# Kernel optimization log

Measured on AMD Instinct MI355X. Metric: run time of the kernel, lower is better.

The kernel has to match this reference:

```python
import jax, jax.numpy as jnp
import numpy as np

N_NODES = 50000
N_EDGES = 800000
D_IN = 64
D_OUT = 64


def setup_inputs() -> dict:
    key = jax.random.key(0)
    k1, k2, k3, k4 = jax.random.split(key, 4)
    x = jax.random.normal(k1, (N_NODES, D_IN), dtype=jnp.float32)
    src = jax.random.randint(k2, (N_EDGES,), 0, N_NODES, dtype=jnp.int64)
    dst = jax.random.randint(k3, (N_EDGES,), 0, N_NODES, dtype=jnp.int64)
    W = jax.random.normal(k4, (D_IN, D_OUT), dtype=jnp.float32) / np.sqrt(D_IN)
    b = jnp.zeros((D_OUT,), dtype=jnp.float32)
    return {"x": x, "src": src, "dst": dst, "W": W, "b": b}


def reference(x, src, dst, W, b):
    # DGL GraphConv, norm='both': out = D_in^{-1/2} A D_out^{-1/2} x W + b
    n = x.shape[0]
    ones = jnp.ones(src.shape[0], dtype=x.dtype)
    out_deg = jax.ops.segment_sum(ones, src, num_segments=n)  # out-degree of each node
    in_deg = jax.ops.segment_sum(ones, dst, num_segments=n)   # in-degree of each node
    norm_src = jax.lax.rsqrt(jnp.clip(out_deg, 1.0))          # [N]
    norm_dst = jax.lax.rsqrt(jnp.clip(in_deg, 1.0))           # [N]
    h = x * norm_src[:, None]                                 # [N, D_in]
    msg = jnp.take(h, src, axis=0)                            # [E, D_in] gather
    agg = jax.ops.segment_sum(msg, dst, num_segments=n)       # [N, D_in] scatter-add
    agg = agg * norm_dst[:, None]
    return agg @ W + b                                        # [N, D_out]
```

## Files before the change

### kernel.cpp

```cpp
#include <hip/hip_runtime.h>
#include <hip/hip_fp16.h>

#define N_NODES 50000
#define N_EDGES 800000
#define D 64

#define SLICES 100
#define I4S    2000
#define NI4    200000
#define NWORDS 12512

typedef float vfloat2 __attribute__((ext_vector_type(2)));

#define CTR_OFF    0
#define META_OFF   256
#define SNORM_OFF  400384
#define SSRC_OFF   600576
#define OCC_OFF    3800576
#define PART_OFF   4600832
#define YA_OFF     14610432
#define YB_OFF     17810688

__global__ __launch_bounds__(256) void degree_occ_kernel(const int4* __restrict__ src4,
                                                         const int4* __restrict__ dst4,
                                                         unsigned int* __restrict__ partial,
                                                         uchar4* __restrict__ occ4,
                                                         int* __restrict__ ctr) {
    __shared__ unsigned int hist[NWORDS];
    int tid = threadIdx.x;
    if (blockIdx.x == 0 && tid == 0) *ctr = 0;
    uint4* h4 = (uint4*)hist;
    for (int i = tid; i < NWORDS / 4; i += 256) h4[i] = make_uint4(0, 0, 0, 0);
    __syncthreads();

    int role  = blockIdx.x & 1;
    int slice = blockIdx.x >> 1;
    int beg = slice * I4S, end = beg + I4S;
    if (role == 0) {
        for (int i = beg + tid; i < end; i += 256) {
            int4 v = src4[i];
            atomicAdd(&hist[v.x >> 2], 1u << ((v.x & 3) * 8));
            atomicAdd(&hist[v.y >> 2], 1u << ((v.y & 3) * 8));
            atomicAdd(&hist[v.z >> 2], 1u << ((v.z & 3) * 8));
            atomicAdd(&hist[v.w >> 2], 1u << ((v.w & 3) * 8));
        }
    } else {
        for (int i = beg + tid; i < end; i += 256) {
            int4 v = dst4[i];
            unsigned int o0 = (atomicAdd(&hist[v.x >> 2], 1u << ((v.x & 3) * 8)) >> ((v.x & 3) * 8)) & 0xFFu;
            unsigned int o1 = (atomicAdd(&hist[v.y >> 2], 1u << ((v.y & 3) * 8)) >> ((v.y & 3) * 8)) & 0xFFu;
            unsigned int o2 = (atomicAdd(&hist[v.z >> 2], 1u << ((v.z & 3) * 8)) >> ((v.z & 3) * 8)) & 0xFFu;
            unsigned int o3 = (atomicAdd(&hist[v.w >> 2], 1u << ((v.w & 3) * 8)) >> ((v.w & 3) * 8)) & 0xFFu;
            occ4[i] = make_uchar4((unsigned char)o0, (unsigned char)o1,
                                  (unsigned char)o2, (unsigned char)o3);
        }
    }
    __syncthreads();

    uint4* p4 = (uint4*)(partial + (size_t)blockIdx.x * NWORDS);
    for (int i = tid; i < NWORDS / 4; i += 256) p4[i] = h4[i];
}

__global__ __launch_bounds__(256) void merge_scan_kernel(unsigned int* __restrict__ partial,
                                                         int2* __restrict__ meta,
                                                         float* __restrict__ snorm,
                                                         int* __restrict__ ctr) {
    int w = blockIdx.x * blockDim.x + threadIdx.x;
    int lane = threadIdx.x & 63;
    unsigned int accin = 0, accout = 0;
    if (w < 12500) {
        unsigned int* po = partial + w;
        unsigned int* pd = partial + NWORDS + w;
#pragma unroll 4
        for (int s = 0; s < SLICES; s++) {
            size_t off = (size_t)(2 * s) * NWORDS;
            accout += po[off];
            unsigned int v = pd[off];
            pd[off] = accin;
            accin += v;
        }
    }
    int d0 = accin & 0xFF, d1 = (accin >> 8) & 0xFF,
        d2 = (accin >> 16) & 0xFF, d3 = (accin >> 24) & 0xFF;
    int tsum = d0 + d1 + d2 + d3;
    int run = tsum;
#pragma unroll
    for (int off = 1; off < 64; off <<= 1) {
        int v = __shfl_up(run, off);
        if (lane >= off) run += v;
    }
    int wtot = __shfl(run, 63);
    int wbase = 0;
    if (lane == 63) wbase = atomicAdd(ctr, wtot);
    wbase = __shfl(wbase, 63);
    if (w < 12500) {
        int b0 = wbase + run - tsum;
        int b1 = b0 + d0, b2 = b1 + d1, b3 = b2 + d2;
        ((int4*)meta)[2 * w]     = make_int4(b0, d0, b1, d1);
        ((int4*)meta)[2 * w + 1] = make_int4(b2, d2, b3, d3);
        int o0 = accout & 0xFF, o1 = (accout >> 8) & 0xFF,
            o2 = (accout >> 16) & 0xFF, o3 = (accout >> 24) & 0xFF;
        ((float4*)snorm)[w] = make_float4(rsqrtf(fmaxf((float)o0, 1.f)),
                                          rsqrtf(fmaxf((float)o1, 1.f)),
                                          rsqrtf(fmaxf((float)o2, 1.f)),
                                          rsqrtf(fmaxf((float)o3, 1.f)));
    }
}

#define FYBLK 1024
__global__ __launch_bounds__(256, 4) void filly_kernel(const int4* __restrict__ src4,
                                                       const int4* __restrict__ dst4,
                                                       const uchar4* __restrict__ occ4,
                                                       const unsigned int* __restrict__ partial,
                                                       const int2* __restrict__ meta,
                                                       int* __restrict__ ssrc,
                                                       const float* __restrict__ x,
                                                       const float* __restrict__ snorm,
                                                       const float* __restrict__ W,
                                                       __half* __restrict__ yA,
                                                       __half* __restrict__ yB) {
    int tid = blockIdx.x * blockDim.x + threadIdx.x;
    int lane = threadIdx.x & 63;

    if (tid < NI4) {
        int s = tid / I4S;
        const unsigned int* pref = partial + (size_t)(2 * s + 1) * NWORDS;
        int4 sv = src4[tid], tv = dst4[tid];
        uchar4 oc = occ4[tid];
#define FILL_ONE(T, S, O)                                                     \
        {                                                                     \
            int t = (T); int sh = (t & 3) * 8;                                \
            int p = meta[t].x + (int)((pref[t >> 2] >> sh) & 0xFFu) + (int)(O); \
            ssrc[p] = (S);                                                    \
        }
        FILL_ONE(tv.x, sv.x, oc.x)
        FILL_ONE(tv.y, sv.y, oc.y)
        FILL_ONE(tv.z, sv.z, oc.z)
        FILL_ONE(tv.w, sv.w, oc.w)
#undef FILL_ONE
    }

    float Wreg[D];
#pragma unroll
    for (int k = 0; k < D; k++) Wreg[k] = W[k * D + lane];
    __half* yh = (lane < 32) ? yA : yB;
    int jl = lane & 31;
    int wave = tid >> 6;
    const int nwaves = FYBLK * 4;
    for (int n = wave; n < N_NODES; n += nwaves) {
        float hv = x[(size_t)n * D + lane] * snorm[n];
        int hb = __float_as_int(hv);
        float p0 = 0.f, p1 = 0.f, p2 = 0.f, p3 = 0.f;
#pragma unroll
        for (int k = 0; k < D; k += 4) {
            p0 = fmaf(__int_as_float(__builtin_amdgcn_readlane(hb, k + 0)), Wreg[k + 0], p0);
            p1 = fmaf(__int_as_float(__builtin_amdgcn_readlane(hb, k + 1)), Wreg[k + 1], p1);
            p2 = fmaf(__int_as_float(__builtin_amdgcn_readlane(hb, k + 2)), Wreg[k + 2], p2);
            p3 = fmaf(__int_as_float(__builtin_amdgcn_readlane(hb, k + 3)), Wreg[k + 3], p3);
        }
        yh[(size_t)n * 32 + jl] = __float2half((p0 + p1) + (p2 + p3));
    }
}

#define GBLK 2048
__global__ __launch_bounds__(256, 8) void gather_kernel(const __half2* __restrict__ yA,
                                                        const __half2* __restrict__ yB,
                                                        const int* __restrict__ ssrc,
                                                        const int2* __restrict__ meta,
                                                        const float* __restrict__ bias,
                                                        float* __restrict__ out) {
    int lane = threadIdx.x & 63;
    int q = lane >> 4;
    int c = lane & 15;
    int pass = blockIdx.x & 1;
    int pblk = blockIdx.x >> 1;
    int wave = (pblk << 2) | (threadIdx.x >> 6);
    const int nwaves = (GBLK / 2) * 4;

    float2 b2 = ((const float2*)bias)[(pass << 4) + c];
    const __half2* ycol = (pass ? yB : yA) + c;

#define ACC(A, F) { (A).x += (F).x; (A).y += (F).y; }

    for (int n = wave; n < N_NODES; n += nwaves) {
        int2 m = meta[n];
        int beg = m.x, end = m.x + m.y;
        float dn = rsqrtf(fmaxf((float)m.y, 1.0f));
        float2 a0 = make_float2(0.f, 0.f), a1 = a0, a2 = a0, a3 = a0;
        float2 a4 = a0, a5 = a0, a6 = a0, a7 = a0;
        int i = beg;
        for (; i + 32 <= end; i += 32) {
            int s0 = ssrc[i + q],      s1 = ssrc[i + 4 + q];
            int s2 = ssrc[i + 8 + q],  s3 = ssrc[i + 12 + q];
            int s4 = ssrc[i + 16 + q], s5 = ssrc[i + 20 + q];
            int s6 = ssrc[i + 24 + q], s7 = ssrc[i + 28 + q];
            float2 f0 = __half22float2(ycol[(size_t)s0 * 16]);
            float2 f1 = __half22float2(ycol[(size_t)s1 * 16]);
            float2 f2 = __half22float2(ycol[(size_t)s2 * 16]);
            float2 f3 = __half22float2(ycol[(size_t)s3 * 16]);
            float2 f4 = __half22float2(ycol[(size_t)s4 * 16]);
            float2 f5 = __half22float2(ycol[(size_t)s5 * 16]);
            float2 f6 = __half22float2(ycol[(size_t)s6 * 16]);
            float2 f7 = __half22float2(ycol[(size_t)s7 * 16]);
            ACC(a0, f0) ACC(a1, f1) ACC(a2, f2) ACC(a3, f3)
            ACC(a4, f4) ACC(a5, f5) ACC(a6, f6) ACC(a7, f7)
        }
        for (; i + 16 <= end; i += 16) {
            int s0 = ssrc[i + q],      s1 = ssrc[i + 4 + q];
            int s2 = ssrc[i + 8 + q],  s3 = ssrc[i + 12 + q];
            float2 f0 = __half22float2(ycol[(size_t)s0 * 16]);
            float2 f1 = __half22float2(ycol[(size_t)s1 * 16]);
            float2 f2 = __half22float2(ycol[(size_t)s2 * 16]);
            float2 f3 = __half22float2(ycol[(size_t)s3 * 16]);
            ACC(a0, f0) ACC(a1, f1) ACC(a2, f2) ACC(a3, f3)
        }
        for (; i + 4 <= end; i += 4) {
            int s = ssrc[i + q];
            float2 f = __half22float2(ycol[(size_t)s * 16]);
            ACC(a0, f)
        }
        int rem = end - i;
        if (q < rem) {
            int s = ssrc[i + q];
            float2 f = __half22float2(ycol[(size_t)s * 16]);
            ACC(a1, f)
        }
        float2 t;
        t.x = ((a0.x + a1.x) + (a2.x + a3.x)) + ((a4.x + a5.x) + (a6.x + a7.x));
        t.y = ((a0.y + a1.y) + (a2.y + a3.y)) + ((a4.y + a5.y) + (a6.y + a7.y));
        t.x += __shfl(t.x, lane ^ 16); t.y += __shfl(t.y, lane ^ 16);
        t.x += __shfl(t.x, lane ^ 32); t.y += __shfl(t.y, lane ^ 32);
        if (q == 0) {
            vfloat2 o;
            o.x = fmaf(t.x, dn, b2.x);
            o.y = fmaf(t.y, dn, b2.y);
            __builtin_nontemporal_store(o, (vfloat2*)(out + (size_t)n * D + (pass << 5)) + c);
        }
    }
#undef ACC
}

extern "C" void kernel_launch(void* const* d_in, const int* in_sizes, int n_in,
                              void* d_out, int out_size, void* d_ws, size_t ws_size,
                              hipStream_t stream) {
    const float* x   = (const float*)d_in[0];
    const int*   src = (const int*)d_in[1];
    const int*   dst = (const int*)d_in[2];
    const float* W   = (const float*)d_in[3];
    const float* b   = (const float*)d_in[4];
    float* out = (float*)d_out;

    char* ws = (char*)d_ws;
    int*          ctr   = (int*)(ws + CTR_OFF);
    int2*         meta  = (int2*)(ws + META_OFF);
    float*        snorm = (float*)(ws + SNORM_OFF);
    int*          ssrc  = (int*)(ws + SSRC_OFF);
    uchar4*       occ4  = (uchar4*)(ws + OCC_OFF);
    unsigned int* part  = (unsigned int*)(ws + PART_OFF);
    __half*       yA    = (__half*)(ws + YA_OFF);
    __half*       yB    = (__half*)(ws + YB_OFF);

    const int4* src4 = (const int4*)src;
    const int4* dst4 = (const int4*)dst;

    degree_occ_kernel<<<2 * SLICES, 256, 0, stream>>>(src4, dst4, part, occ4, ctr);
    merge_scan_kernel<<<(12500 + 255) / 256, 256, 0, stream>>>(part, meta, snorm, ctr);
    filly_kernel<<<FYBLK, 256, 0, stream>>>(src4, dst4, occ4, part, meta, ssrc,
                                            x, snorm, W, yA, yB);
    gather_kernel<<<GBLK, 256, 0, stream>>>((const __half2*)yA, (const __half2*)yB,
                                            ssrc, meta, b, out);
}
```

Before: 151.6 us.

## Overlap x@W with degree histogram and move source norm into gather

The x@W projection no longer depends on the source degree norm. The per-source norm is now applied inside the gather as an FMA weight, which lets the projection run in extra blocks of the degree/histogram kernel at the same time as the histogramming. The merge-scan kernel now uses 4 threads per word, splitting the 100-slice prefix scan into halves across in and out, to get more parallelism. The cost is an extra snorm gather per edge in the gather kernel and a lone projection that competes for the same launch as the LDS-heavy histogram blocks.

```diff
diff --git a/kernel.cpp b/kernel.cpp
--- a/kernel.cpp
+++ b/kernel.cpp
@@ -9,6 +9,9 @@
 #define I4S    2000
 #define NI4    200000
 #define NWORDS 12512
+#define HBLK   200
+#define ZBLK   568
+#define DEGZ_BLOCKS (HBLK + ZBLK)
 
 typedef float vfloat2 __attribute__((ext_vector_type(2)));
 
@@ -18,16 +21,46 @@
 #define SSRC_OFF   600576
 #define OCC_OFF    3800576
 #define PART_OFF   4600832
-#define YA_OFF     14610432
-#define YB_OFF     17810688
-
-__global__ __launch_bounds__(256) void degree_occ_kernel(const int4* __restrict__ src4,
-                                                         const int4* __restrict__ dst4,
-                                                         unsigned int* __restrict__ partial,
-                                                         uchar4* __restrict__ occ4,
-                                                         int* __restrict__ ctr) {
+#define ZA_OFF     14610432
+#define ZB_OFF     17810688
+
+__global__ __launch_bounds__(256) void degz_kernel(const int4* __restrict__ src4,
+                                                   const int4* __restrict__ dst4,
+                                                   unsigned int* __restrict__ partial,
+                                                   uchar4* __restrict__ occ4,
+                                                   int* __restrict__ ctr,
+                                                   const float* __restrict__ x,
+                                                   const float* __restrict__ W,
+                                                   __half* __restrict__ zA,
+                                                   __half* __restrict__ zB) {
     __shared__ unsigned int hist[NWORDS];
     int tid = threadIdx.x;
+
+    if (blockIdx.x >= HBLK) {
+        int lane = tid & 63;
+        float Wreg[D];
+#pragma unroll
+        for (int k = 0; k < D; k++) Wreg[k] = W[k * D + lane];
+        __half* zh = (lane < 32) ? zA : zB;
+        int jl = lane & 31;
+        int wave = (blockIdx.x - HBLK) * 4 + (tid >> 6);
+        const int nwaves = ZBLK * 4;
+        for (int n = wave; n < N_NODES; n += nwaves) {
+            float hv = x[(size_t)n * D + lane];
+            int hb = __float_as_int(hv);
+            float p0 = 0.f, p1 = 0.f, p2 = 0.f, p3 = 0.f;
+#pragma unroll
+            for (int k = 0; k < D; k += 4) {
+                p0 = fmaf(__int_as_float(__builtin_amdgcn_readlane(hb, k + 0)), Wreg[k + 0], p0);
+                p1 = fmaf(__int_as_float(__builtin_amdgcn_readlane(hb, k + 1)), Wreg[k + 1], p1);
+                p2 = fmaf(__int_as_float(__builtin_amdgcn_readlane(hb, k + 2)), Wreg[k + 2], p2);
+                p3 = fmaf(__int_as_float(__builtin_amdgcn_readlane(hb, k + 3)), Wreg[k + 3], p3);
+            }
+            zh[(size_t)n * 32 + jl] = __float2half((p0 + p1) + (p2 + p3));
+        }
+        return;
+    }
+
     if (blockIdx.x == 0 && tid == 0) *ctr = 0;
     uint4* h4 = (uint4*)hist;
     for (int i = tid; i < NWORDS / 4; i += 256) h4[i] = make_uint4(0, 0, 0, 0);
@@ -61,29 +94,55 @@
     for (int i = tid; i < NWORDS / 4; i += 256) p4[i] = h4[i];
 }
 
+#define MSBLK 196
 __global__ __launch_bounds__(256) void merge_scan_kernel(unsigned int* __restrict__ partial,
                                                          int2* __restrict__ meta,
                                                          float* __restrict__ snorm,
                                                          int* __restrict__ ctr) {
-    int w = blockIdx.x * blockDim.x + threadIdx.x;
     int lane = threadIdx.x & 63;
-    unsigned int accin = 0, accout = 0;
-    if (w < 12500) {
-        unsigned int* po = partial + w;
-        unsigned int* pd = partial + NWORDS + w;
-#pragma unroll 4
-        for (int s = 0; s < SLICES; s++) {
-            size_t off = (size_t)(2 * s) * NWORDS;
-            accout += po[off];
-            unsigned int v = pd[off];
-            pd[off] = accin;
-            accin += v;
-        }
-    }
+    int r = threadIdx.x & 3;
+    int w = (blockIdx.x * blockDim.x + threadIdx.x) >> 2;
+    bool act = (w < 12500);
+
+    unsigned int buf[50];
+    unsigned int acc = 0;
+    if (act) {
+        int isdst = (r >= 2);
+        int sbase = (r & 1) ? 50 : 0;
+        unsigned int* p = partial + (size_t)isdst * NWORDS
+                        + (size_t)(2 * sbase) * NWORDS + w;
+#pragma unroll
+        for (int s = 0; s < 50; s++) {
+            unsigned int v = p[(size_t)(2 * s) * NWORDS];
+            buf[s] = v;
+            if (r == 2) p[(size_t)(2 * s) * NWORDS] = acc;
+            acc += v;
+        }
+    }
+    unsigned int mysum = acc;
+
+    int wl = lane & ~3;
+    unsigned int s0v = __shfl(mysum, wl);
+    unsigned int s1v = __shfl(mysum, wl | 1);
+    unsigned int s2v = __shfl(mysum, wl | 2);
+    unsigned int s3v = __shfl(mysum, wl | 3);
+
+    if (act && r == 3) {
+        unsigned int* p = partial + NWORDS + (size_t)(2 * 50) * NWORDS + w;
+        unsigned int a2 = s2v;
+#pragma unroll
+        for (int s = 0; s < 50; s++) {
+            p[(size_t)(2 * s) * NWORDS] = a2;
+            a2 += buf[s];
+        }
+    }
+
+    unsigned int accin  = s2v + s3v;
+    unsigned int accout = s0v + s1v;
     int d0 = accin & 0xFF, d1 = (accin >> 8) & 0xFF,
         d2 = (accin >> 16) & 0xFF, d3 = (accin >> 24) & 0xFF;
     int tsum = d0 + d1 + d2 + d3;
-    int run = tsum;
+    int run = (act && r == 3) ? tsum : 0;
 #pragma unroll
     for (int off = 1; off < 64; off <<= 1) {
         int v = __shfl_up(run, off);
@@ -93,7 +152,8 @@
     int wbase = 0;
     if (lane == 63) wbase = atomicAdd(ctr, wtot);
     wbase = __shfl(wbase, 63);
-    if (w < 12500) {
+
+    if (act && r == 3) {
         int b0 = wbase + run - tsum;
         int b1 = b0 + d0, b2 = b1 + d1, b3 = b2 + d2;
         ((int4*)meta)[2 * w]     = make_int4(b0, d0, b1, d1);
@@ -107,66 +167,37 @@
     }
 }
 
-#define FYBLK 1024
-__global__ __launch_bounds__(256, 4) void filly_kernel(const int4* __restrict__ src4,
-                                                       const int4* __restrict__ dst4,
-                                                       const uchar4* __restrict__ occ4,
-                                                       const unsigned int* __restrict__ partial,
-                                                       const int2* __restrict__ meta,
-                                                       int* __restrict__ ssrc,
-                                                       const float* __restrict__ x,
-                                                       const float* __restrict__ snorm,
-                                                       const float* __restrict__ W,
-                                                       __half* __restrict__ yA,
-                                                       __half* __restrict__ yB) {
+__global__ __launch_bounds__(256) void fill_kernel(const int4* __restrict__ src4,
+                                                   const int4* __restrict__ dst4,
+                                                   const uchar4* __restrict__ occ4,
+                                                   const unsigned int* __restrict__ partial,
+                                                   const int2* __restrict__ meta,
+                                                   int* __restrict__ ssrc) {
     int tid = blockIdx.x * blockDim.x + threadIdx.x;
-    int lane = threadIdx.x & 63;
-
-    if (tid < NI4) {
-        int s = tid / I4S;
-        const unsigned int* pref = partial + (size_t)(2 * s + 1) * NWORDS;
-        int4 sv = src4[tid], tv = dst4[tid];
-        uchar4 oc = occ4[tid];
+    if (tid >= NI4) return;
+    int s = tid / I4S;
+    const unsigned int* pref = partial + (size_t)(2 * s + 1) * NWORDS;
+    int4 sv = src4[tid], tv = dst4[tid];
+    uchar4 oc = occ4[tid];
 #define FILL_ONE(T, S, O)                                                     \
-        {                                                                     \
-            int t = (T); int sh = (t & 3) * 8;                                \
-            int p = meta[t].x + (int)((pref[t >> 2] >> sh) & 0xFFu) + (int)(O); \
-            ssrc[p] = (S);                                                    \
-        }
-        FILL_ONE(tv.x, sv.x, oc.x)
-        FILL_ONE(tv.y, sv.y, oc.y)
-        FILL_ONE(tv.z, sv.z, oc.z)
-        FILL_ONE(tv.w, sv.w, oc.w)
+    {                                                                         \
+        int t = (T); int sh = (t & 3) * 8;                                    \
+        int p = meta[t].x + (int)((pref[t >> 2] >> sh) & 0xFFu) + (int)(O);   \
+        ssrc[p] = (S);                                                        \
+    }
+    FILL_ONE(tv.x, sv.x, oc.x)
+    FILL_ONE(tv.y, sv.y, oc.y)
+    FILL_ONE(tv.z, sv.z, oc.z)
+    FILL_ONE(tv.w, sv.w, oc.w)
 #undef FILL_ONE
-    }
-
-    float Wreg[D];
-#pragma unroll
-    for (int k = 0; k < D; k++) Wreg[k] = W[k * D + lane];
-    __half* yh = (lane < 32) ? yA : yB;
-    int jl = lane & 31;
-    int wave = tid >> 6;
-    const int nwaves = FYBLK * 4;
-    for (int n = wave; n < N_NODES; n += nwaves) {
-        float hv = x[(size_t)n * D + lane] * snorm[n];
-        int hb = __float_as_int(hv);
-        float p0 = 0.f, p1 = 0.f, p2 = 0.f, p3 = 0.f;
-#pragma unroll
-        for (int k = 0; k < D; k += 4) {
-            p0 = fmaf(__int_as_float(__builtin_amdgcn_readlane(hb, k + 0)), Wreg[k + 0], p0);
-            p1 = fmaf(__int_as_float(__builtin_amdgcn_readlane(hb, k + 1)), Wreg[k + 1], p1);
-            p2 = fmaf(__int_as_float(__builtin_amdgcn_readlane(hb, k + 2)), Wreg[k + 2], p2);
-            p3 = fmaf(__int_as_float(__builtin_amdgcn_readlane(hb, k + 3)), Wreg[k + 3], p3);
-        }
-        yh[(size_t)n * 32 + jl] = __float2half((p0 + p1) + (p2 + p3));
-    }
 }
 
 #define GBLK 2048
-__global__ __launch_bounds__(256, 8) void gather_kernel(const __half2* __restrict__ yA,
-                                                        const __half2* __restrict__ yB,
+__global__ __launch_bounds__(256, 8) void gather_kernel(const __half2* __restrict__ zA,
+                                                        const __half2* __restrict__ zB,
                                                         const int* __restrict__ ssrc,
                                                         const int2* __restrict__ meta,
+                                                        const float* __restrict__ snorm,
                                                         const float* __restrict__ bias,
                                                         float* __restrict__ out) {
     int lane = threadIdx.x & 63;
@@ -178,9 +209,9 @@
     const int nwaves = (GBLK / 2) * 4;
 
     float2 b2 = ((const float2*)bias)[(pass << 4) + c];
-    const __half2* ycol = (pass ? yB : yA) + c;
-
-#define ACC(A, F) { (A).x += (F).x; (A).y += (F).y; }
+    const __half2* zcol = (pass ? zB : zA) + c;
+
+#define ACC(A, F, SN) { (A).x = fmaf((F).x, (SN), (A).x); (A).y = fmaf((F).y, (SN), (A).y); }
 
     for (int n = wave; n < N_NODES; n += nwaves) {
         int2 m = meta[n];
@@ -194,36 +225,41 @@
             int s2 = ssrc[i + 8 + q],  s3 = ssrc[i + 12 + q];
             int s4 = ssrc[i + 16 + q], s5 = ssrc[i + 20 + q];
             int s6 = ssrc[i + 24 + q], s7 = ssrc[i + 28 + q];
-            float2 f0 = __half22float2(ycol[(size_t)s0 * 16]);
-            float2 f1 = __half22float2(ycol[(size_t)s1 * 16]);
-            float2 f2 = __half22float2(ycol[(size_t)s2 * 16]);
-            float2 f3 = __half22float2(ycol[(size_t)s3 * 16]);
-            float2 f4 = __half22float2(ycol[(size_t)s4 * 16]);
-            float2 f5 = __half22float2(ycol[(size_t)s5 * 16]);
-            float2 f6 = __half22float2(ycol[(size_t)s6 * 16]);
-            float2 f7 = __half22float2(ycol[(size_t)s7 * 16]);
-            ACC(a0, f0) ACC(a1, f1) ACC(a2, f2) ACC(a3, f3)
-            ACC(a4, f4) ACC(a5, f5) ACC(a6, f6) ACC(a7, f7)
+            float n0 = snorm[s0], n1 = snorm[s1], n2 = snorm[s2], n3 = snorm[s3];
+            float n4 = snorm[s4], n5 = snorm[s5], n6 = snorm[s6], n7 = snorm[s7];
+            float2 f0 = __half22float2(zcol[(size_t)s0 * 16]);
+            float2 f1 = __half22float2(zcol[(size_t)s1 * 16]);
+            float2 f2 = __half22float2(zcol[(size_t)s2 * 16]);
+            float2 f3 = __half22float2(zcol[(size_t)s3 * 16]);
+            float2 f4 = __half22float2(zcol[(size_t)s4 * 16]);
+            float2 f5 = __half22float2(zcol[(size_t)s5 * 16]);
+            float2 f6 = __half22float2(zcol[(size_t)s6 * 16]);
+            float2 f7 = __half22float2(zcol[(size_t)s7 * 16]);
+            ACC(a0, f0, n0) ACC(a1, f1, n1) ACC(a2, f2, n2) ACC(a3, f3, n3)
+            ACC(a4, f4, n4) ACC(a5, f5, n5) ACC(a6, f6, n6) ACC(a7, f7, n7)
         }
         for (; i + 16 <= end; i += 16) {
             int s0 = ssrc[i + q],      s1 = ssrc[i + 4 + q];
             int s2 = ssrc[i + 8 + q],  s3 = ssrc[i + 12 + q];
-            float2 f0 = __half22float2(ycol[(size_t)s0 * 16]);
-            float2 f1 = __half22float2(ycol[(size_t)s1 * 16]);
-            float2 f2 = __half22float2(ycol[(size_t)s2 * 16]);
-            float2 f3 = __half22float2(ycol[(size_t)s3 * 16]);
-            ACC(a0, f0) ACC(a1, f1) ACC(a2, f2) ACC(a3, f3)
+            float n0 = snorm[s0], n1 = snorm[s1], n2 = snorm[s2], n3 = snorm[s3];
+            float2 f0 = __half22float2(zcol[(size_t)s0 * 16]);
+            float2 f1 = __half22float2(zcol[(size_t)s1 * 16]);
+            float2 f2 = __half22float2(zcol[(size_t)s2 * 16]);
+            float2 f3 = __half22float2(zcol[(size_t)s3 * 16]);
+            ACC(a0, f0, n0) ACC(a1, f1, n1) ACC(a2, f2, n2) ACC(a3, f3, n3)
         }
         for (; i + 4 <= end; i += 4) {
             int s = ssrc[i + q];
-            float2 f = __half22float2(ycol[(size_t)s * 16]);
-            ACC(a0, f)
+            float sn = snorm[s];
+            float2 f = __half22float2(zcol[(size_t)s * 16]);
+            ACC(a0, f, sn)
         }
         int rem = end - i;
         if (q < rem) {
             int s = ssrc[i + q];
-            float2 f = __half22float2(ycol[(size_t)s * 16]);
-            ACC(a1, f)
+            float sn = snorm[s];
+            float2 f = __half22float2(zcol[(size_t)s * 16]);
+            ACC(a1, f, sn)
         }
         float2 t;
         t.x = ((a0.x + a1.x) + (a2.x + a3.x)) + ((a4.x + a5.x) + (a6.x + a7.x));
@@ -257,16 +293,17 @@
     int*          ssrc  = (int*)(ws + SSRC_OFF);
     uchar4*       occ4  = (uchar4*)(ws + OCC_OFF);
     unsigned int* part  = (unsigned int*)(ws + PART_OFF);
-    __half*       yA    = (__half*)(ws + YA_OFF);
-    __half*       yB    = (__half*)(ws + YB_OFF);
+    __half*       zA    = (__half*)(ws + ZA_OFF);
+    __half*       zB    = (__half*)(ws + ZB_OFF);
 
     const int4* src4 = (const int4*)src;
     const int4* dst4 = (const int4*)dst;
 
-    degree_occ_kernel<<<2 * SLICES, 256, 0, stream>>>(src4, dst4, part, occ4, ctr);
-    merge_scan_kernel<<<(12500 + 255) / 256, 256, 0, stream>>>(part, meta, snorm, ctr);
-    filly_kernel<<<FYBLK, 256, 0, stream>>>(src4, dst4, occ4, part, meta, ssrc,
-                                            x, snorm, W, yA, yB);
-    gather_kernel<<<GBLK, 256, 0, stream>>>((const __half2*)yA, (const __half2*)yB,
-                                            ssrc, meta, b, out);
-}
+    degz_kernel<<<DEGZ_BLOCKS, 256, 0, stream>>>(src4, dst4, part, occ4, ctr,
+                                                 x, W, zA, zB);
+    merge_scan_kernel<<<MSBLK, 256, 0, stream>>>(part, meta, snorm, ctr);
+    fill_kernel<<<(NI4 + 255) / 256, 256, 0, stream>>>(src4, dst4, occ4, part,
+                                                       meta, ssrc);
+    gather_kernel<<<GBLK, 256, 0, stream>>>((const __half2*)zA, (const __half2*)zB,
+                                            ssrc, meta, snorm, b, out);
+}
```

Measured after the change: 175.9 us. 1.16x slower.
